# Kernel optimization log

Measured on AMD Instinct MI355X. Metric: run time of the kernel, lower is better.

## Reference

```python
import jax, jax.numpy as jnp
import numpy as np

N_NODES = 100000
N_EDGES = 1600000


def gcn_conv(h_in, row, col, W, b, num_nodes):
    """PyG-style GCNConv: linear transform, add self-loops, symmetric
    deg^{-1/2} normalization, scatter-add aggregation at target nodes."""
    h = h_in @ W  # [N, out]
    loops = jnp.arange(num_nodes, dtype=row.dtype)
    r = jnp.concatenate([row, loops])  # source
    c = jnp.concatenate([col, loops])  # target
    ew = jnp.ones(r.shape[0], dtype=h.dtype)
    deg = jax.ops.segment_sum(ew, c, num_segments=num_nodes)  # in-degree incl. self-loop
    dinv = jnp.where(deg > 0, jax.lax.rsqrt(deg), 0.0)
    norm = dinv[r] * dinv[c]  # [E+N]
    msgs = norm[:, None] * h[r]  # gather + scale, [E+N, out]
    out = jax.ops.segment_sum(msgs, c, num_segments=num_nodes)  # scatter-add
    return out + b


def setup_inputs() -> dict:
    key = jax.random.key(0)
    ks = jax.random.split(key, 8)
    in_f, hid, out_f = 128, 128, 64
    x = jax.random.normal(ks[0], (N_NODES, in_f), dtype=jnp.float32)
    edge_index = jax.random.randint(ks[1], (2, N_EDGES), 0, N_NODES, dtype=jnp.int64)
    edge_weight = jax.random.uniform(ks[2], (N_EDGES,), dtype=jnp.float32)
    s1 = 1.0 / np.sqrt(in_f)
    s2 = 1.0 / np.sqrt(hid)
    s3 = 1.0 / np.sqrt(out_f)
    W1 = jax.random.normal(ks[3], (in_f, hid), dtype=jnp.float32) * s1
    b1 = jnp.zeros((hid,), dtype=jnp.float32)
    W2 = jax.random.normal(ks[4], (hid, out_f), dtype=jnp.float32) * s2
    b2 = jnp.zeros((out_f,), dtype=jnp.float32)
    Wfc = jax.random.normal(ks[5], (out_f, 1), dtype=jnp.float32) * s3
    bfc = jnp.zeros((1,), dtype=jnp.float32)
    return {"x": x, "edge_index": edge_index, "edge_weight": edge_weight,
            "W1": W1, "b1": b1, "W2": W2, "b2": b2, "Wfc": Wfc, "bfc": bfc}


def reference(x, edge_index, edge_weight, W1, b1, W2, b2, Wfc, bfc):
    # eval mode: dropout(p=0.6) is identity; edge_weight is unused by the
    # original forward (edge_attr never passed to GCNConv).
    row, col = edge_index[0], edge_index[1]
    n = x.shape[0]
    h = jax.nn.relu(gcn_conv(x, row, col, W1, b1, n))
    h = gcn_conv(h, row, col, W2, b2, n)
    return h @ Wfc + bfc  # [N, 1]
```

## Files before the change

### kernel.cpp

```cpp
#include <hip/hip_runtime.h>
#include <cstddef>

#define CAP 64
#define BK_SHIFT 8
#define BSTRIDE 8192
#define CHUNK 2048

typedef unsigned int uint32;
typedef unsigned short ushort;
typedef __attribute__((ext_vector_type(8))) short short8;
typedef __attribute__((ext_vector_type(4))) float f32x4;

__device__ __forceinline__ float bf_lo(uint32 v) {
  union { uint32 u; float f; } c; c.u = v << 16; return c.f;
}
__device__ __forceinline__ float bf_hi(uint32 v) {
  union { uint32 u; float f; } c; c.u = v & 0xffff0000u; return c.f;
}
__device__ __forceinline__ uint32 pack_bf2(float a, float b) {
  union { float f; uint32 u; } x, y; x.f = a; y.f = b;
  uint32 ua = x.u + 0x7fffu + ((x.u >> 16) & 1u);
  uint32 ub = y.u + 0x7fffu + ((y.u >> 16) & 1u);
  return (ua >> 16) | (ub & 0xffff0000u);
}
__device__ __forceinline__ ushort bf16_1(float x) {
  union { float f; uint32 u; } c; c.f = x;
  return (ushort)((c.u + 0x7fffu + ((c.u >> 16) & 1u)) >> 16);
}

union ABu { uint32 u[4]; short8 v; };

__global__ void k_zero(int* __restrict__ p, int n) {
  int i = blockIdx.x * blockDim.x + threadIdx.x;
  if (i < n) p[i] = 0;
}

__global__ __launch_bounds__(256) void k_part1(const int* __restrict__ ei,
                                               int* __restrict__ bcnt,
                                               int* __restrict__ stage,
                                               int E, int N, int NB) {
  __shared__ int hist[512];
  __shared__ int gbase[512];
  const int tid = threadIdx.x;
  const int base = blockIdx.x * CHUNK;
  for (int b = tid; b < NB; b += 256) hist[b] = 0;
  __syncthreads();
  int rr[8], cc[8], lp[8];
  #pragma unroll
  for (int j = 0; j < 8; j++) {
    int e = base + tid + j * 256;
    int r = -1, c = -1;
    if (e < E) { r = ei[e]; c = ei[(size_t)E + e]; }
    bool ok = ((unsigned)r < (unsigned)N) && ((unsigned)c < (unsigned)N);
    rr[j] = ok ? r : -1;
    cc[j] = c;
    lp[j] = ok ? atomicAdd(&hist[c >> BK_SHIFT], 1) : 0;
  }
  __syncthreads();
  for (int b = tid; b < NB; b += 256) {
    int h = hist[b];
    gbase[b] = h ? atomicAdd(&bcnt[b], h) : 0;
  }
  __syncthreads();
  #pragma unroll
  for (int j = 0; j < 8; j++) {
    if (rr[j] >= 0) {
      int b = cc[j] >> BK_SHIFT;
      int pos = gbase[b] + lp[j];
      if (pos < BSTRIDE)
        stage[(size_t)b * BSTRIDE + pos] = (rr[j] << 8) | (cc[j] & 255);
    }
  }
}

__global__ __launch_bounds__(256) void k_fill2(const int* __restrict__ stage,
                                               const int* __restrict__ bcnt,
                                               int* __restrict__ csr,
                                               int* __restrict__ cnt,
                                               float* __restrict__ dinv, int N) {
  __shared__ int lc[256];
  const int b = blockIdx.x;
  const int tid = threadIdx.x;
  lc[tid] = 0;
  __syncthreads();
  int m = bcnt[b]; if (m > BSTRIDE) m = BSTRIDE;
  const int node0 = b << BK_SHIFT;
  const int* __restrict__ sb = stage + (size_t)b * BSTRIDE;
  for (int e = tid; e < m; e += 256) {
    int v = sb[e];
    int cl = v & 255;
    int r = v >> 8;
    int pos = atomicAdd(&lc[cl], 1);
    if (pos < CAP) csr[(size_t)(node0 + cl) * CAP + pos] = r;
  }
  __syncthreads();
  int node = node0 + tid;
  if (node < N) {
    int d = lc[tid]; if (d > CAP) d = CAP;
    cnt[node] = d;
    int d8 = (d + 7) & ~7; if (d8 > CAP) d8 = CAP;
    for (int p = d; p < d8; p++) csr[(size_t)node * CAP + p] = node;
    dinv[node] = rsqrtf((float)(lc[tid] + 1));
  }
}

__global__ void k_wc(const float* __restrict__ W2, const float* __restrict__ Wfc,
                     const float* __restrict__ b2, const float* __restrict__ bfc,
                     float* __restrict__ wv, float* __restrict__ c0) {
  int k = threadIdx.x;
  float s = 0.f;
  #pragma unroll 8
  for (int j = 0; j < 64; j++) s += W2[k * 64 + j] * Wfc[j];
  wv[k] = s;
  if (k == 0) {
    float cc = 0.f;
    for (int j = 0; j < 64; j++) cc += b2[j] * Wfc[j];
    c0[0] = cc + bfc[0];
  }
}

__global__ __launch_bounds__(256) void k_gemm(const float* __restrict__ X,
                                              const float* __restrict__ W,
                                              const float* __restrict__ dinv,
                                              ushort* __restrict__ Xh, int M) {
  __shared__ ushort WtT[16384];
  const int tid  = threadIdx.x;
  const int lane = tid & 63;
  const int wv   = tid >> 6;
  const int cl   = lane & 15;
  const int g    = lane >> 4;

  const int rb = blockIdx.x * 64 + wv * 16;

  int rowc = rb + cl; if (rowc >= M) rowc = M - 1;
  const float* xr = X + (size_t)rowc * 128;
  ABu af[4];
  #pragma unroll
  for (int kk = 0; kk < 4; kk++) {
    float4 p = *(const float4*)&xr[kk * 32 + g * 8];
    float4 q = *(const float4*)&xr[kk * 32 + g * 8 + 4];
    af[kk].u[0] = pack_bf2(p.x, p.y);
    af[kk].u[1] = pack_bf2(p.z, p.w);
    af[kk].u[2] = pack_bf2(q.x, q.y);
    af[kk].u[3] = pack_bf2(q.z, q.w);
  }

  float dvr[4];
  #pragma unroll
  for (int r = 0; r < 4; r++) {
    int rw = rb + g * 4 + r; if (rw >= M) rw = M - 1;
    dvr[r] = dinv[rw];
  }

  for (int idx = tid; idx < 8192; idx += 256) {
    int k = idx >> 6;
    int c = (idx & 63) * 2;
    float2 w2 = *(const float2*)&W[k * 128 + c];
    int gr = ((k >> 3) ^ ((c & 15) >> 1)) & 15;
    int base = (gr << 4) + (k & 7) * 2;
    *(ushort*)((char*)WtT + c * 256 + base)       = bf16_1(w2.x);
    *(ushort*)((char*)WtT + (c + 1) * 256 + base) = bf16_1(w2.y);
  }
  __syncthreads();

  #pragma unroll
  for (int ct = 0; ct < 8; ct++) {
    const char* wrow = (const char*)WtT + (ct * 16 + cl) * 256;
    f32x4 acc = {0.f, 0.f, 0.f, 0.f};
    #pragma unroll
    for (int kk = 0; kk < 4; kk++) {
      int grn = ((4 * kk + g) ^ (cl >> 1)) & 15;
      short8 bfrag = *(const short8*)(wrow + (grn << 4));
      acc = __builtin_amdgcn_mfma_f32_16x16x32_bf16(af[kk].v, bfrag, acc, 0, 0, 0);
    }
    #pragma unroll
    for (int r = 0; r < 4; r++) {
      int rw = rb + g * 4 + r;
      if (rw < M) Xh[(size_t)rw * 128 + ct * 16 + cl] = bf16_1(dvr[r] * acc[r]);
    }
  }
}

__global__ __launch_bounds__(256) void k_agg1(const uint32* __restrict__ Xh,
                                              const int* __restrict__ csr,
                                              const int* __restrict__ cnt,
                                              const float* __restrict__ dinv,
                                              const float* __restrict__ b1,
                                              const float* __restrict__ wv,
                                              float* __restrict__ dz, int N) {
  int wid = (blockIdx.x * 256 + threadIdx.x) >> 6;
  int lane = threadIdx.x & 63;
  if (wid >= N) return;
  const int i = wid;
  int deg = cnt[i]; if (deg > CAP) deg = CAP;
  const int deg8 = (deg + 7) & ~7;
  const float di = dinv[i];
  const int edge_reg = csr[(size_t)i * CAP + lane];

  uint32 vs = Xh[(size_t)i * 64 + lane];
  float a0x = 0.f, a0y = 0.f, a1x = 0.f, a1y = 0.f;
  float a2x = 0.f, a2y = 0.f, a3x = 0.f, a3y = 0.f;
  float a4x = 0.f, a4y = 0.f, a5x = 0.f, a5y = 0.f;
  float a6x = 0.f, a6y = 0.f, a7x = 0.f, a7y = 0.f;

  for (int e = 0; e < deg8; e += 8) {
    int s0 = __builtin_amdgcn_readlane(edge_reg, e + 0);
    int s1 = __builtin_amdgcn_readlane(edge_reg, e + 1);
    int s2 = __builtin_amdgcn_readlane(edge_reg, e + 2);
    int s3 = __builtin_amdgcn_readlane(edge_reg, e + 3);
    int s4 = __builtin_amdgcn_readlane(edge_reg, e + 4);
    int s5 = __builtin_amdgcn_readlane(edge_reg, e + 5);
    int s6 = __builtin_amdgcn_readlane(edge_reg, e + 6);
    int s7 = __builtin_amdgcn_readlane(edge_reg, e + 7);
    uint32 v0 = Xh[(size_t)s0 * 64 + lane];
    uint32 v1 = Xh[(size_t)s1 * 64 + lane];
    uint32 v2 = Xh[(size_t)s2 * 64 + lane];
    uint32 v3 = Xh[(size_t)s3 * 64 + lane];
    uint32 v4 = Xh[(size_t)s4 * 64 + lane];
    uint32 v5 = Xh[(size_t)s5 * 64 + lane];
    uint32 v6 = Xh[(size_t)s6 * 64 + lane];
    uint32 v7 = Xh[(size_t)s7 * 64 + lane];
    a0x += bf_lo(v0); a0y += bf_hi(v0);
    a1x += bf_lo(v1); a1y += bf_hi(v1);
    a2x += bf_lo(v2); a2y += bf_hi(v2);
    a3x += bf_lo(v3); a3y += bf_hi(v3);
    a4x += bf_lo(v4); a4y += bf_hi(v4);
    a5x += bf_lo(v5); a5y += bf_hi(v5);
    a6x += bf_lo(v6); a6y += bf_hi(v6);
    a7x += bf_lo(v7); a7y += bf_hi(v7);
  }
  const float selfc = 1.0f - (float)(deg8 - deg);
  float sx = ((a0x + a1x) + (a2x + a3x)) + ((a4x + a5x) + (a6x + a7x));
  float sy = ((a0y + a1y) + (a2y + a3y)) + ((a4y + a5y) + (a6y + a7y));
  sx = fmaf(selfc, bf_lo(vs), sx);
  sy = fmaf(selfc, bf_hi(vs), sy);

  float2 bb = *(const float2*)&b1[lane * 2];
  float h0 = fmaxf(fmaf(di, sx, bb.x), 0.f);
  float h1 = fmaxf(fmaf(di, sy, bb.y), 0.f);
  float2 ww = *(const float2*)&wv[lane * 2];
  float part = fmaf(h0, ww.x, h1 * ww.y);
  #pragma unroll
  for (int m = 32; m > 0; m >>= 1) part += __shfl_xor(part, m, 64);
  if (lane == 0) dz[i] = di * part;
}

__global__ __launch_bounds__(256) void k_out(const float* __restrict__ dz,
                                             const int* __restrict__ csr,
                                             const int* __restrict__ cnt,
                                             const float* __restrict__ dinv,
                                             const float* __restrict__ c0,
                                             float* __restrict__ out, int N) {
  int i = blockIdx.x * 256 + threadIdx.x;
  if (i >= N) return;
  int deg = cnt[i]; if (deg > CAP) deg = CAP;
  const int* __restrict__ edges = csr + (size_t)i * CAP;
  float s0 = dz[i], s1 = 0.f, s2 = 0.f, s3 = 0.f;
  int e = 0;
  for (; e + 4 <= deg; e += 4) {
    int i0 = edges[e + 0], i1 = edges[e + 1], i2 = edges[e + 2], i3 = edges[e + 3];
    s0 += dz[i0]; s1 += dz[i1]; s2 += dz[i2]; s3 += dz[i3];
  }
  for (; e < deg; e++) s0 += dz[edges[e]];
  out[i] = dinv[i] * ((s0 + s1) + (s2 + s3)) + c0[0];
}

extern "C" void kernel_launch(void* const* d_in, const int* in_sizes, int n_in,
                              void* d_out, int out_size, void* d_ws, size_t ws_size,
                              hipStream_t stream) {
  const float* x   = (const float*)d_in[0];
  const int*   ei  = (const int*)d_in[1];
  const float* W1  = (const float*)d_in[3];
  const float* b1  = (const float*)d_in[4];
  const float* W2  = (const float*)d_in[5];
  const float* b2  = (const float*)d_in[6];
  const float* Wfc = (const float*)d_in[7];
  const float* bfc = (const float*)d_in[8];
  float* out = (float*)d_out;

  const int N = in_sizes[0] / 128;
  const int E = in_sizes[1] / 2;
  const int NB = (N + 255) >> 8;

  char* ws = (char*)d_ws;
  ushort* Xh  = (ushort*)(ws);
  int*   stage= (int*)   (ws);
  int*   csr  = (int*)   (ws + (size_t)N * 256);
  int*   cnt  = (int*)   (ws + (size_t)N * 512);
  float* dinv = (float*) (ws + (size_t)N * 516);
  float* dz   = (float*) (ws + (size_t)N * 520);
  int*   bcnt = (int*)dz;
  float* wv   = (float*) (ws + (size_t)N * 524);
  float* c0   = wv + 128;

  hipLaunchKernelGGL(k_zero,  dim3((NB + 255) / 256), dim3(256), 0, stream, bcnt, NB);
  hipLaunchKernelGGL(k_part1, dim3((E + CHUNK - 1) / CHUNK), dim3(256), 0, stream,
                     ei, bcnt, stage, E, N, NB);
  hipLaunchKernelGGL(k_fill2, dim3(NB), dim3(256), 0, stream,
                     stage, bcnt, csr, cnt, dinv, N);
  hipLaunchKernelGGL(k_gemm,  dim3((N + 63) / 64), dim3(256), 0, stream,
                     x, W1, dinv, Xh, N);
  hipLaunchKernelGGL(k_wc,    dim3(1), dim3(128), 0, stream, W2, Wfc, b2, bfc, wv, c0);
  hipLaunchKernelGGL(k_agg1,  dim3(((size_t)N * 64 + 255) / 256), dim3(256), 0, stream,
                     (const uint32*)Xh, csr, cnt, dinv, b1, wv, dz, N);
  hipLaunchKernelGGL(k_out,   dim3((N + 255) / 256), dim3(256), 0, stream,
                     dz, csr, cnt, dinv, c0, out, N);
}
```

Measured before the change: 161.3 us.

## Fold k_wc into k_fill2, memset counters, add nontemporal loads, vectorize k_out

Removes two small kernel launches: the bucket-count zeroing becomes a hipMemsetAsync, and the W2·Wfc projection runs in an extra block of k_fill2. Streaming reads of edge indices, staging, X and CSR use nontemporal loads to avoid polluting the cache. k_out now reads CSR in int4 vectors over the self-padded degree and subtracts the padding contribution from the self term, and k_agg1 loads CSR entries only for lanes within the padded degree. These trade small launch and load-instruction costs for extra branching and reliance on the self-index padding layout.

```diff
diff --git a/kernel.cpp b/kernel.cpp
--- a/kernel.cpp
+++ b/kernel.cpp
@@ -10,6 +10,8 @@
 typedef unsigned short ushort;
 typedef __attribute__((ext_vector_type(8))) short short8;
 typedef __attribute__((ext_vector_type(4))) float f32x4;
+typedef __attribute__((ext_vector_type(4))) int int4v;
+typedef __attribute__((ext_vector_type(4))) float float4v;
 
 __device__ __forceinline__ float bf_lo(uint32 v) {
   union { uint32 u; float f; } c; c.u = v << 16; return c.f;
@@ -29,11 +31,6 @@
 }
 
 union ABu { uint32 u[4]; short8 v; };
-
-__global__ void k_zero(int* __restrict__ p, int n) {
-  int i = blockIdx.x * blockDim.x + threadIdx.x;
-  if (i < n) p[i] = 0;
-}
 
 __global__ __launch_bounds__(256) void k_part1(const int* __restrict__ ei,
                                                int* __restrict__ bcnt,
@@ -50,7 +47,10 @@
   for (int j = 0; j < 8; j++) {
     int e = base + tid + j * 256;
     int r = -1, c = -1;
-    if (e < E) { r = ei[e]; c = ei[(size_t)E + e]; }
+    if (e < E) {
+      r = __builtin_nontemporal_load(&ei[e]);
+      c = __builtin_nontemporal_load(&ei[(size_t)E + e]);
+    }
     bool ok = ((unsigned)r < (unsigned)N) && ((unsigned)c < (unsigned)N);
     rr[j] = ok ? r : -1;
     cc[j] = c;
@@ -77,17 +77,37 @@
                                                const int* __restrict__ bcnt,
                                                int* __restrict__ csr,
                                                int* __restrict__ cnt,
-                                               float* __restrict__ dinv, int N) {
-  __shared__ int lc[256];
+                                               float* __restrict__ dinv, int N, int NB,
+                                               const float* __restrict__ W2,
+                                               const float* __restrict__ Wfc,
+                                               const float* __restrict__ b2,
+                                               const float* __restrict__ bfc,
+                                               float* __restrict__ wvo,
+                                               float* __restrict__ c0) {
   const int b = blockIdx.x;
   const int tid = threadIdx.x;
+  if (b == NB) {
+    if (tid < 128) {
+      float s = 0.f;
+      #pragma unroll 8
+      for (int j = 0; j < 64; j++) s += W2[tid * 64 + j] * Wfc[j];
+      wvo[tid] = s;
+      if (tid == 0) {
+        float cc = 0.f;
+        for (int j = 0; j < 64; j++) cc += b2[j] * Wfc[j];
+        c0[0] = cc + bfc[0];
+      }
+    }
+    return;
+  }
+  __shared__ int lc[256];
   lc[tid] = 0;
   __syncthreads();
   int m = bcnt[b]; if (m > BSTRIDE) m = BSTRIDE;
   const int node0 = b << BK_SHIFT;
   const int* __restrict__ sb = stage + (size_t)b * BSTRIDE;
   for (int e = tid; e < m; e += 256) {
-    int v = sb[e];
+    int v = __builtin_nontemporal_load(&sb[e]);
     int cl = v & 255;
     int r = v >> 8;
     int pos = atomicAdd(&lc[cl], 1);
@@ -101,21 +121,6 @@
     int d8 = (d + 7) & ~7; if (d8 > CAP) d8 = CAP;
     for (int p = d; p < d8; p++) csr[(size_t)node * CAP + p] = node;
     dinv[node] = rsqrtf((float)(lc[tid] + 1));
-  }
-}
-
-__global__ void k_wc(const float* __restrict__ W2, const float* __restrict__ Wfc,
-                     const float* __restrict__ b2, const float* __restrict__ bfc,
-                     float* __restrict__ wv, float* __restrict__ c0) {
-  int k = threadIdx.x;
-  float s = 0.f;
-  #pragma unroll 8
-  for (int j = 0; j < 64; j++) s += W2[k * 64 + j] * Wfc[j];
-  wv[k] = s;
-  if (k == 0) {
-    float cc = 0.f;
-    for (int j = 0; j < 64; j++) cc += b2[j] * Wfc[j];
-    c0[0] = cc + bfc[0];
   }
 }
 
@@ -137,8 +142,8 @@
   ABu af[4];
   #pragma unroll
   for (int kk = 0; kk < 4; kk++) {
-    float4 p = *(const float4*)&xr[kk * 32 + g * 8];
-    float4 q = *(const float4*)&xr[kk * 32 + g * 8 + 4];
+    float4v p = __builtin_nontemporal_load((const float4v*)&xr[kk * 32 + g * 8]);
+    float4v q = __builtin_nontemporal_load((const float4v*)&xr[kk * 32 + g * 8 + 4]);
     af[kk].u[0] = pack_bf2(p.x, p.y);
     af[kk].u[1] = pack_bf2(p.z, p.w);
     af[kk].u[2] = pack_bf2(q.x, q.y);
@@ -195,7 +200,8 @@
   int deg = cnt[i]; if (deg > CAP) deg = CAP;
   const int deg8 = (deg + 7) & ~7;
   const float di = dinv[i];
-  const int edge_reg = csr[(size_t)i * CAP + lane];
+  int edge_reg = i;
+  if (lane < deg8) edge_reg = __builtin_nontemporal_load(&csr[(size_t)i * CAP + lane]);
 
   uint32 vs = Xh[(size_t)i * 64 + lane];
   float a0x = 0.f, a0y = 0.f, a1x = 0.f, a1y = 0.f;
@@ -254,14 +260,16 @@
   int i = blockIdx.x * 256 + threadIdx.x;
   if (i >= N) return;
   int deg = cnt[i]; if (deg > CAP) deg = CAP;
-  const int* __restrict__ edges = csr + (size_t)i * CAP;
-  float s0 = dz[i], s1 = 0.f, s2 = 0.f, s3 = 0.f;
-  int e = 0;
-  for (; e + 4 <= deg; e += 4) {
-    int i0 = edges[e + 0], i1 = edges[e + 1], i2 = edges[e + 2], i3 = edges[e + 3];
-    s0 += dz[i0]; s1 += dz[i1]; s2 += dz[i2]; s3 += dz[i3];
-  }
-  for (; e < deg; e++) s0 += dz[edges[e]];
+  const int deg8 = (deg + 7) & ~7;
+  const int4v* __restrict__ edges = (const int4v*)(csr + (size_t)i * CAP);
+  float s0 = (1.0f - (float)(deg8 - deg)) * dz[i];
+  float s1 = 0.f, s2 = 0.f, s3 = 0.f;
+  for (int e4 = 0; e4 < (deg8 >> 2); e4 += 2) {
+    int4v q0 = __builtin_nontemporal_load(&edges[e4]);
+    int4v q1 = __builtin_nontemporal_load(&edges[e4 + 1]);
+    s0 += dz[q0.x]; s1 += dz[q0.y]; s2 += dz[q0.z]; s3 += dz[q0.w];
+    s0 += dz[q1.x]; s1 += dz[q1.y]; s2 += dz[q1.z]; s3 += dz[q1.w];
+  }
   out[i] = dinv[i] * ((s0 + s1) + (s2 + s3)) + c0[0];
 }
 
@@ -293,14 +301,13 @@
   float* wv   = (float*) (ws + (size_t)N * 524);
   float* c0   = wv + 128;
 
-  hipLaunchKernelGGL(k_zero,  dim3((NB + 255) / 256), dim3(256), 0, stream, bcnt, NB);
+  hipMemsetAsync(bcnt, 0, (size_t)NB * 4, stream);
   hipLaunchKernelGGL(k_part1, dim3((E + CHUNK - 1) / CHUNK), dim3(256), 0, stream,
                      ei, bcnt, stage, E, N, NB);
-  hipLaunchKernelGGL(k_fill2, dim3(NB), dim3(256), 0, stream,
-                     stage, bcnt, csr, cnt, dinv, N);
+  hipLaunchKernelGGL(k_fill2, dim3(NB + 1), dim3(256), 0, stream,
+                     stage, bcnt, csr, cnt, dinv, N, NB, W2, Wfc, b2, bfc, wv, c0);
   hipLaunchKernelGGL(k_gemm,  dim3((N + 63) / 64), dim3(256), 0, stream,
                      x, W1, dinv, Xh, N);
-  hipLaunchKernelGGL(k_wc,    dim3(1), dim3(128), 0, stream, W2, Wfc, b2, bfc, wv, c0);
   hipLaunchKernelGGL(k_agg1,  dim3(((size_t)N * 64 + 255) / 256), dim3(256), 0, stream,
                      (const uint32*)Xh, csr, cnt, dinv, b1, wv, dz, N);
   hipLaunchKernelGGL(k_out,   dim3((N + 255) / 256), dim3(256), 0, stream,
```

Result: no change. 161.9 us (+0.4%).
